# Optimization experiments

Measured on AMD Instinct MI355X. Metric: run time of the kernel, lower is better.

Reference implementation:

```python
import jax, jax.numpy as jnp
import numpy as np


def setup_inputs() -> dict:
    key = jax.random.key(0)
    k1, k2, k3, k4, k5 = jax.random.split(key, 5)
    N, IN, OUT = 4096, 2048, 2048
    return {
        "input": jax.random.normal(k1, (N, IN), dtype=jnp.float32),
        "weight_mu": jax.random.normal(k2, (OUT, IN), dtype=jnp.float32) * 0.25,
        "weight_rho": jax.random.normal(k3, (OUT, IN), dtype=jnp.float32) - 5.0,
        "eps_weight": jax.random.normal(k4, (OUT, IN), dtype=jnp.float32),
        "bias": jax.random.normal(k5, (OUT,), dtype=jnp.float32) * 0.02,
    }


def reference(input, weight_mu, weight_rho, eps_weight, bias):
    # Effective weight: mu + softplus(rho) * eps   (log1p(exp(rho)) == softplus)
    w = weight_mu + jax.nn.softplus(weight_rho) * eps_weight  # [out, in]
    # F.linear: input @ w.T + bias
    return jnp.einsum("ni,oi->no", input, w) + bias
```

## Files before the change

kernel.cpp:

```cpp
#include <hip/hip_runtime.h>
#include <stdint.h>

typedef __bf16 bf16x8 __attribute__((ext_vector_type(8)));
typedef float f32x4 __attribute__((ext_vector_type(4)));
typedef float float4v __attribute__((ext_vector_type(4)));
typedef unsigned short u16x8 __attribute__((ext_vector_type(8)));

__device__ __forceinline__ unsigned short f2bf(float f) {
    unsigned u = __float_as_uint(f);
    u += 0x7fffu + ((u >> 16) & 1u);
    return (unsigned short)(u >> 16);
}

__device__ __forceinline__ float softplus(float x) {
    return fmaxf(x, 0.0f) + __logf(1.0f + __expf(-fabsf(x)));
}

__device__ __forceinline__ void gl_lds16(const void* gptr, void* lptr) {
    auto g = reinterpret_cast<const __attribute__((address_space(1))) void*>(
        reinterpret_cast<uintptr_t>(gptr));
    auto l = reinterpret_cast<__attribute__((address_space(3))) void*>(
        reinterpret_cast<uintptr_t>(lptr));
    __builtin_amdgcn_global_load_lds(g, l, 16, 0, 0);
}

__global__ void prep_kernel(const float* __restrict__ in,
                            const float* __restrict__ mu,
                            const float* __restrict__ rho,
                            const float* __restrict__ eps,
                            unsigned short* __restrict__ in_bf,
                            unsigned short* __restrict__ w_bf,
                            int nIn8, int nW8) {
    int i = blockIdx.x * blockDim.x + threadIdx.x;
    if (i < nIn8) {
        const float4v* p = (const float4v*)in + (size_t)i * 2;
        float4v a = p[0], b = p[1];
        u16x8 r;
        r[0] = f2bf(a[0]); r[1] = f2bf(a[1]); r[2] = f2bf(a[2]); r[3] = f2bf(a[3]);
        r[4] = f2bf(b[0]); r[5] = f2bf(b[1]); r[6] = f2bf(b[2]); r[7] = f2bf(b[3]);
        ((u16x8*)in_bf)[i] = r;
    } else {
        int j = i - nIn8;
        if (j >= nW8) return;
        const float4v* pm = (const float4v*)mu  + (size_t)j * 2;
        const float4v* pr = (const float4v*)rho + (size_t)j * 2;
        const float4v* pe = (const float4v*)eps + (size_t)j * 2;
        float4v m0 = pm[0], m1 = pm[1];
        float4v r0 = pr[0], r1 = pr[1];
        float4v e0 = pe[0], e1 = pe[1];
        u16x8 r;
        r[0] = f2bf(m0[0] + softplus(r0[0]) * e0[0]);
        r[1] = f2bf(m0[1] + softplus(r0[1]) * e0[1]);
        r[2] = f2bf(m0[2] + softplus(r0[2]) * e0[2]);
        r[3] = f2bf(m0[3] + softplus(r0[3]) * e0[3]);
        r[4] = f2bf(m1[0] + softplus(r1[0]) * e1[0]);
        r[5] = f2bf(m1[1] + softplus(r1[1]) * e1[1]);
        r[6] = f2bf(m1[2] + softplus(r1[2]) * e1[2]);
        r[7] = f2bf(m1[3] + softplus(r1[3]) * e1[3]);
        ((u16x8*)w_bf)[j] = r;
    }
}

#define BM 128
#define BN 128
#define BK 64
#define EX_S 66

__global__ __launch_bounds__(512, 4)
void gemm_bt_kernel(const unsigned short* __restrict__ A,
                    const unsigned short* __restrict__ B,
                    const float* __restrict__ bias,
                    float* __restrict__ C,
                    int M, int N, int K) {
    __shared__ unsigned short smem[32768];
    unsigned short* lds_a0 = smem;
    unsigned short* lds_b0 = smem + 16384;

    const int t      = threadIdx.x;
    const int lane   = t & 63;
    const int wave   = t >> 6;
    const int lane16 = lane & 15;
    const int quad   = lane >> 4;
    const int wq     = wave & 3;
    const int kh     = wave >> 2;
    const int wm     = wq & 1;
    const int wn     = wq >> 1;

    const int m0 = blockIdx.y * BM;
    const int n0 = blockIdx.x * BN;

    const int r1   = t >> 3;
    const int pkg1 = t & 7;
    const int g1   = (pkg1 ^ (r1 & 7)) * 8;
    const int r2   = r1 + 64;
    const int g2   = (pkg1 ^ (r2 & 7)) * 8;

    const unsigned short* Ab = A + (size_t)m0 * K;
    const unsigned short* Bb = B + (size_t)n0 * K;

    f32x4 acc[4][4] = {};

    auto stage = [&](int buf, int k0) {
        gl_lds16(Ab + (size_t)r1 * K + k0 + g1, lds_a0 + buf * 8192 + t * 8);
        gl_lds16(Ab + (size_t)r2 * K + k0 + g2, lds_a0 + buf * 8192 + 4096 + t * 8);
        gl_lds16(Bb + (size_t)r1 * K + k0 + g1, lds_b0 + buf * 8192 + t * 8);
        gl_lds16(Bb + (size_t)r2 * K + k0 + g2, lds_b0 + buf * 8192 + 4096 + t * 8);
    };

    const int sw = lane16 & 7;
    const int raBase = (wm * 64 + lane16) * BK + (((kh * 4 + quad) ^ sw) * 8);
    const int rbBase = (wn * 64 + lane16) * BK + (((kh * 4 + quad) ^ sw) * 8);

    const int nit = K / BK;
    stage(0, 0);
    __syncthreads();

    auto body = [&](int cur, int it) {
        const unsigned short* la = lds_a0 + cur * 8192;
        const unsigned short* lb = lds_b0 + cur * 8192;
        bf16x8 af[4], bfr[4];
#pragma unroll
        for (int mi = 0; mi < 4; ++mi)
            af[mi] = *(const bf16x8*)(la + raBase + mi * 16 * BK);
#pragma unroll
        for (int ni = 0; ni < 4; ++ni)
            bfr[ni] = *(const bf16x8*)(lb + rbBase + ni * 16 * BK);
        if (it + 1 < nit) stage(cur ^ 1, (it + 1) * BK);
#pragma unroll
        for (int mi = 0; mi < 4; ++mi)
#pragma unroll
            for (int ni = 0; ni < 4; ++ni)
                acc[mi][ni] = __builtin_amdgcn_mfma_f32_16x16x32_bf16(
                    af[mi], bfr[ni], acc[mi][ni], 0, 0, 0);
        __syncthreads();
    };

    for (int it = 0; it < nit; it += 2) {
        body(0, it);
        body(1, it + 1);
    }

    float* fs = (float*)smem;
#pragma unroll
    for (int ph = 0; ph < 2; ++ph) {
        const bool mine = (wq >> 1) == ph;
        const int rbase0 = (wq & 1) * (64 * EX_S);
        if (kh == 1 && mine) {
#pragma unroll
            for (int mi = 0; mi < 4; ++mi)
#pragma unroll
                for (int ni = 0; ni < 4; ++ni)
#pragma unroll
                    for (int rr = 0; rr < 4; ++rr)
                        fs[rbase0 + (mi * 16 + quad * 4 + rr) * EX_S +
                           ni * 16 + lane16] = acc[mi][ni][rr];
        }
        __syncthreads();
        if (kh == 0 && mine) {
#pragma unroll
            for (int mi = 0; mi < 4; ++mi)
#pragma unroll
                for (int ni = 0; ni < 4; ++ni)
#pragma unroll
                    for (int rr = 0; rr < 4; ++rr)
                        acc[mi][ni][rr] += fs[rbase0 +
                            (mi * 16 + quad * 4 + rr) * EX_S + ni * 16 + lane16];
        }
        __syncthreads();
    }

    if (kh != 0) return;

    float bv[4];
#pragma unroll
    for (int ni = 0; ni < 4; ++ni)
        bv[ni] = bias[n0 + wn * 64 + ni * 16 + lane16];

#pragma unroll
    for (int mi = 0; mi < 4; ++mi) {
        const int rbase = m0 + wm * 64 + mi * 16 + quad * 4;
#pragma unroll
        for (int ni = 0; ni < 4; ++ni) {
            const int col = n0 + wn * 64 + ni * 16 + lane16;
#pragma unroll
            for (int rr = 0; rr < 4; ++rr)
                C[(size_t)(rbase + rr) * N + col] = acc[mi][ni][rr] + bv[ni];
        }
    }
}

extern "C" void kernel_launch(void* const* d_in, const int* in_sizes, int n_in,
                              void* d_out, int out_size, void* d_ws, size_t ws_size,
                              hipStream_t stream) {
    const float* input = (const float*)d_in[0];
    const float* mu    = (const float*)d_in[1];
    const float* rho   = (const float*)d_in[2];
    const float* eps   = (const float*)d_in[3];
    const float* bias  = (const float*)d_in[4];
    float* out = (float*)d_out;

    const int OUT = in_sizes[4];
    const int IN  = in_sizes[1] / OUT;
    const int M   = in_sizes[0] / IN;

    unsigned short* in_bf = (unsigned short*)d_ws;
    unsigned short* w_bf  = in_bf + (size_t)M * IN;

    const int nIn8 = (M * IN) / 8;
    const int nW8  = (OUT * IN) / 8;
    prep_kernel<<<dim3((nIn8 + nW8 + 255) / 256), 256, 0, stream>>>(
        input, mu, rho, eps, in_bf, w_bf, nIn8, nW8);

    gemm_bt_kernel<<<dim3(OUT / BN, M / BM), 512, 0, stream>>>(
        in_bf, w_bf, bias, out, M, OUT, IN);
}
```

Baseline: 159.3 us.

## Fuse input bf16 conversion into GEMM A-tile loading and swizzle block order

The fp32 input is no longer converted to bf16 by the prep kernel. The GEMM now loads fp32 A tiles into registers, converts them, and writes them to LDS after the MFMA phase, while W keeps its async global-to-LDS path. This removes a full write and re-read of the 16 MB bf16 input copy, but each A tile is re-read in fp32 by all 16 column blocks, which doubles A load bandwidth and adds register pressure. The block index is also remapped so that neighbouring workgroups share tiles, for better L2 reuse.

```diff
diff --git a/kernel.cpp b/kernel.cpp
--- a/kernel.cpp
+++ b/kernel.cpp
@@ -24,41 +24,29 @@
     __builtin_amdgcn_global_load_lds(g, l, 16, 0, 0);
 }
 
-__global__ void prep_kernel(const float* __restrict__ in,
-                            const float* __restrict__ mu,
+__global__ void prep_kernel(const float* __restrict__ mu,
                             const float* __restrict__ rho,
                             const float* __restrict__ eps,
-                            unsigned short* __restrict__ in_bf,
                             unsigned short* __restrict__ w_bf,
-                            int nIn8, int nW8) {
-    int i = blockIdx.x * blockDim.x + threadIdx.x;
-    if (i < nIn8) {
-        const float4v* p = (const float4v*)in + (size_t)i * 2;
-        float4v a = p[0], b = p[1];
-        u16x8 r;
-        r[0] = f2bf(a[0]); r[1] = f2bf(a[1]); r[2] = f2bf(a[2]); r[3] = f2bf(a[3]);
-        r[4] = f2bf(b[0]); r[5] = f2bf(b[1]); r[6] = f2bf(b[2]); r[7] = f2bf(b[3]);
-        ((u16x8*)in_bf)[i] = r;
-    } else {
-        int j = i - nIn8;
-        if (j >= nW8) return;
-        const float4v* pm = (const float4v*)mu  + (size_t)j * 2;
-        const float4v* pr = (const float4v*)rho + (size_t)j * 2;
-        const float4v* pe = (const float4v*)eps + (size_t)j * 2;
-        float4v m0 = pm[0], m1 = pm[1];
-        float4v r0 = pr[0], r1 = pr[1];
-        float4v e0 = pe[0], e1 = pe[1];
-        u16x8 r;
-        r[0] = f2bf(m0[0] + softplus(r0[0]) * e0[0]);
-        r[1] = f2bf(m0[1] + softplus(r0[1]) * e0[1]);
-        r[2] = f2bf(m0[2] + softplus(r0[2]) * e0[2]);
-        r[3] = f2bf(m0[3] + softplus(r0[3]) * e0[3]);
-        r[4] = f2bf(m1[0] + softplus(r1[0]) * e1[0]);
-        r[5] = f2bf(m1[1] + softplus(r1[1]) * e1[1]);
-        r[6] = f2bf(m1[2] + softplus(r1[2]) * e1[2]);
-        r[7] = f2bf(m1[3] + softplus(r1[3]) * e1[3]);
-        ((u16x8*)w_bf)[j] = r;
-    }
+                            int nW8) {
+    int j = blockIdx.x * blockDim.x + threadIdx.x;
+    if (j >= nW8) return;
+    const float4v* pm = (const float4v*)mu  + (size_t)j * 2;
+    const float4v* pr = (const float4v*)rho + (size_t)j * 2;
+    const float4v* pe = (const float4v*)eps + (size_t)j * 2;
+    float4v m0 = pm[0], m1 = pm[1];
+    float4v r0 = pr[0], r1 = pr[1];
+    float4v e0 = pe[0], e1 = pe[1];
+    u16x8 r;
+    r[0] = f2bf(m0[0] + softplus(r0[0]) * e0[0]);
+    r[1] = f2bf(m0[1] + softplus(r0[1]) * e0[1]);
+    r[2] = f2bf(m0[2] + softplus(r0[2]) * e0[2]);
+    r[3] = f2bf(m0[3] + softplus(r0[3]) * e0[3]);
+    r[4] = f2bf(m1[0] + softplus(r1[0]) * e1[0]);
+    r[5] = f2bf(m1[1] + softplus(r1[1]) * e1[1]);
+    r[6] = f2bf(m1[2] + softplus(r1[2]) * e1[2]);
+    r[7] = f2bf(m1[3] + softplus(r1[3]) * e1[3]);
+    ((u16x8*)w_bf)[j] = r;
 }
 
 #define BM 128
@@ -67,8 +55,8 @@
 #define EX_S 66
 
 __global__ __launch_bounds__(512, 4)
-void gemm_bt_kernel(const unsigned short* __restrict__ A,
-                    const unsigned short* __restrict__ B,
+void gemm_bt_kernel(const float* __restrict__ A,
+                    const unsigned short* __restrict__ W,
                     const float* __restrict__ bias,
                     float* __restrict__ C,
                     int M, int N, int K) {
@@ -86,8 +74,10 @@
     const int wm     = wq & 1;
     const int wn     = wq >> 1;
 
-    const int m0 = blockIdx.y * BM;
-    const int n0 = blockIdx.x * BN;
+    const int orig = blockIdx.y * gridDim.x + blockIdx.x;
+    const int swz  = ((orig & 7) << 6) | (orig >> 3);
+    const int m0 = (swz >> 4) * BM;
+    const int n0 = (swz & 15) * BN;
 
     const int r1   = t >> 3;
     const int pkg1 = t & 7;
@@ -95,16 +85,33 @@
     const int r2   = r1 + 64;
     const int g2   = (pkg1 ^ (r2 & 7)) * 8;
 
-    const unsigned short* Ab = A + (size_t)m0 * K;
-    const unsigned short* Bb = B + (size_t)n0 * K;
+    const float*          Af = A + (size_t)m0 * K;
+    const unsigned short* Wb = W + (size_t)n0 * K;
 
     f32x4 acc[4][4] = {};
-
-    auto stage = [&](int buf, int k0) {
-        gl_lds16(Ab + (size_t)r1 * K + k0 + g1, lds_a0 + buf * 8192 + t * 8);
-        gl_lds16(Ab + (size_t)r2 * K + k0 + g2, lds_a0 + buf * 8192 + 4096 + t * 8);
-        gl_lds16(Bb + (size_t)r1 * K + k0 + g1, lds_b0 + buf * 8192 + t * 8);
-        gl_lds16(Bb + (size_t)r2 * K + k0 + g2, lds_b0 + buf * 8192 + 4096 + t * 8);
+    float4v ald[4];
+
+    auto stageB = [&](int buf, int k0) {
+        gl_lds16(Wb + (size_t)r1 * K + k0 + g1, lds_b0 + buf * 8192 + t * 8);
+        gl_lds16(Wb + (size_t)r2 * K + k0 + g2, lds_b0 + buf * 8192 + 4096 + t * 8);
+    };
+    auto issueA = [&](int k0) {
+        const float4v* p1 = (const float4v*)(Af + (size_t)r1 * K + k0 + g1);
+        const float4v* p2 = (const float4v*)(Af + (size_t)r2 * K + k0 + g2);
+        ald[0] = p1[0]; ald[1] = p1[1];
+        ald[2] = p2[0]; ald[3] = p2[1];
+    };
+    auto writeA = [&](int buf) {
+        u16x8 w0, w1;
+#pragma unroll
+        for (int j = 0; j < 4; ++j) {
+            w0[j]     = f2bf(ald[0][j]);
+            w0[j + 4] = f2bf(ald[1][j]);
+            w1[j]     = f2bf(ald[2][j]);
+            w1[j + 4] = f2bf(ald[3][j]);
+        }
+        *(u16x8*)(lds_a0 + buf * 8192 + t * 8)        = w0;
+        *(u16x8*)(lds_a0 + buf * 8192 + 4096 + t * 8) = w1;
     };
 
     const int sw = lane16 & 7;
@@ -112,7 +119,9 @@
     const int rbBase = (wn * 64 + lane16) * BK + (((kh * 4 + quad) ^ sw) * 8);
 
     const int nit = K / BK;
-    stage(0, 0);
+    issueA(0);
+    stageB(0, 0);
+    writeA(0);
     __syncthreads();
 
     auto body = [&](int cur, int it) {
@@ -125,13 +134,17 @@
 #pragma unroll
         for (int ni = 0; ni < 4; ++ni)
             bfr[ni] = *(const bf16x8*)(lb + rbBase + ni * 16 * BK);
-        if (it + 1 < nit) stage(cur ^ 1, (it + 1) * BK);
+        if (it + 1 < nit) {
+            stageB(cur ^ 1, (it + 1) * BK);
+            issueA((it + 1) * BK);
+        }
 #pragma unroll
         for (int mi = 0; mi < 4; ++mi)
 #pragma unroll
             for (int ni = 0; ni < 4; ++ni)
                 acc[mi][ni] = __builtin_amdgcn_mfma_f32_16x16x32_bf16(
                     af[mi], bfr[ni], acc[mi][ni], 0, 0, 0);
+        if (it + 1 < nit) writeA(cur ^ 1);
         __syncthreads();
     };
 
@@ -203,14 +216,12 @@
     const int IN  = in_sizes[1] / OUT;
     const int M   = in_sizes[0] / IN;
 
-    unsigned short* in_bf = (unsigned short*)d_ws;
-    unsigned short* w_bf  = in_bf + (size_t)M * IN;
-
-    const int nIn8 = (M * IN) / 8;
-    const int nW8  = (OUT * IN) / 8;
-    prep_kernel<<<dim3((nIn8 + nW8 + 255) / 256), 256, 0, stream>>>(
-        input, mu, rho, eps, in_bf, w_bf, nIn8, nW8);
+    unsigned short* w_bf = (unsigned short*)d_ws;
+
+    const int nW8 = (OUT * IN) / 8;
+    prep_kernel<<<dim3((nW8 + 255) / 256), 256, 0, stream>>>(
+        mu, rho, eps, w_bf, nW8);
 
     gemm_bt_kernel<<<dim3(OUT / BN, M / BM), 512, 0, stream>>>(
-        in_bf, w_bf, bias, out, M, OUT, IN);
-}
+        input, w_bf, bias, out, M, OUT, IN);
+}
```

New measurement: 198.2 us. 24.4% more time.
